# Kernel tuning notes

Measured on AMD Instinct MI355X. Metric: run time of the kernel, lower is better.

## Reference

```python
import jax, jax.numpy as jnp
import numpy as np

N, E, DIN, DOUT = 50000, 800000, 256, 256
P = DOUT // 2  # attention projection dim = feature_dim // 2


def _mlp2(x, W1, b1, W2, b2):
    # nn.Sequential(Linear, ReLU, Linear)
    return jax.nn.relu(x @ W1 + b1) @ W2 + b2


def _spmm(indices, values, x):
    # y[r] = sum_e values[e] * x[col[e]] for edges with row[e] == r
    rows, cols = indices[0], indices[1]
    return jax.ops.segment_sum(values[:, None] * x[cols], rows, num_segments=x.shape[0])


def setup_inputs() -> dict:
    key = jax.random.key(0)
    ks = iter(jax.random.split(key, 64))

    def nrm(shape, scale=0.05):
        return jax.random.normal(next(ks), shape, jnp.float32) * scale

    inp = {}
    inp["features"] = jax.random.normal(next(ks), (N, DIN), jnp.float32)
    inp["edge_features"] = jax.random.normal(next(ks), (N, DOUT), jnp.float32)
    for i in (1, 2, 3, 4):
        inp[f"adj{i}_indices"] = jax.random.randint(next(ks), (2, E), 0, N)
        inp[f"adj{i}_values"] = jax.random.uniform(next(ks), (E,), jnp.float32)
    # feature_transform: Linear(in, out)
    inp["ft_W"] = nrm((DIN, DOUT)); inp["ft_b"] = jnp.zeros((DOUT,), jnp.float32)
    # six 2-layer MLPs: first_order(fo), edge(em), second(so), third(to), fourth(qo), final(m)
    for p in ("fo", "em", "so", "to", "qo", "m"):
        inp[f"{p}_W1"] = nrm((DOUT, DOUT)); inp[f"{p}_b1"] = jnp.zeros((DOUT,), jnp.float32)
        inp[f"{p}_W2"] = nrm((DOUT, DOUT)); inp[f"{p}_b2"] = jnp.zeros((DOUT,), jnp.float32)
    # attention query/key projections to DOUT//2
    inp["q_W"] = nrm((DOUT, P)); inp["q_b"] = jnp.zeros((P,), jnp.float32)
    inp["k_W"] = nrm((DOUT, P)); inp["k_b"] = jnp.zeros((P,), jnp.float32)
    return inp


def reference(features, edge_features,
              adj1_indices, adj1_values, adj2_indices, adj2_values,
              adj3_indices, adj3_values, adj4_indices, adj4_values,
              ft_W, ft_b,
              fo_W1, fo_b1, fo_W2, fo_b2,
              em_W1, em_b1, em_W2, em_b2,
              so_W1, so_b1, so_W2, so_b2,
              to_W1, to_b1, to_W2, to_b2,
              qo_W1, qo_b1, qo_W2, qo_b2,
              m_W1, m_b1, m_W2, m_b2,
              q_W, q_b, k_W, k_b):
    feats = features @ ft_W + ft_b                                    # [N, DOUT]
    # first order: spmm -> MLP, then add spmm of edge-MLP features
    fo = _mlp2(_spmm(adj1_indices, adj1_values, feats), fo_W1, fo_b1, fo_W2, fo_b2)
    ef = _mlp2(edge_features, em_W1, em_b1, em_W2, em_b2)
    fo = fo + _spmm(adj1_indices, adj1_values, ef)
    # higher orders: spmm -> MLP + residual
    so_agg = _spmm(adj2_indices, adj2_values, feats)
    so = _mlp2(so_agg, so_W1, so_b1, so_W2, so_b2) + so_agg
    to_agg = _spmm(adj3_indices, adj3_values, feats)
    to = _mlp2(to_agg, to_W1, to_b1, to_W2, to_b2) + to_agg
    qo_agg = _spmm(adj4_indices, adj4_values, feats)
    qo = _mlp2(qo_agg, qo_W1, qo_b1, qo_W2, qo_b2) + qo_agg
    # attention combination over the 5 feature sets
    all_f = jnp.stack([feats, fo, so, to, qo], axis=1)                # [N, 5, DOUT]
    q = feats @ q_W + q_b                                             # [N, P]
    keys = all_f @ k_W + k_b                                          # [N, 5, P]
    scores = jnp.einsum('np,nkp->nk', q, keys)                        # [N, 5]
    w = jax.nn.softmax(scores, axis=-1)
    combined = jnp.einsum('nk,nkd->nd', w, all_f)                     # [N, DOUT]
    # final MLP (dropout is identity in eval mode)
    return _mlp2(combined, m_W1, m_b1, m_W2, m_b2)
```

## Files before the change

kernel.cpp:

```cpp
#include <hip/hip_runtime.h>


#define DO 256

typedef unsigned short u16;
typedef _Float16 f16;
typedef __attribute__((ext_vector_type(8))) _Float16 f16x8;
typedef __attribute__((ext_vector_type(4))) _Float16 f16x4;
typedef __attribute__((ext_vector_type(4))) float f32x4;


struct WDesc { const float* src; f16* dst; };
struct WPack { WDesc w[13]; };
struct CsrSrc { const int* rows[4]; const int* cols[4]; const float* vals[4]; int E[4]; };

__global__ __launch_bounds__(256) void prep_kernel(
    CsrSrc cs, int* __restrict__ cnt, int NPo, WPack wp,
    const float* __restrict__ qW, const float* __restrict__ kW,
    const float* __restrict__ qb, f16* __restrict__ pdst, float* __restrict__ pb)
{
    int y = blockIdx.y;
    if (y < 4) {
        int e = blockIdx.x * 256 + threadIdx.x;
        if (e < cs.E[y]) atomicAdd(&cnt[(size_t)y * NPo + cs.rows[y][e]], 1);
        return;
    }
    if (y < 17) {
        if (blockIdx.x >= 256) return;
        WDesc d = wp.w[y - 4];
        int idx = blockIdx.x * 256 + threadIdx.x;
        int e  = idx & 7;
        int l  = (idx >> 3) & 63;
        int ks = (idx >> 9) & 7;
        int f  = idx >> 12;
        int c  = (f << 4) | (l & 15);
        int k  = ks * 32 + ((l >> 4) << 3) + e;
        d.dst[idx] = (f16)d.src[k * 256 + c];
        return;
    }
    if (y == 17) {
        if (blockIdx.x >= 256) return;
        int idx = blockIdx.x * 256 + threadIdx.x;
        int e  = idx & 7;
        int l  = (idx >> 3) & 63;
        int ks = (idx >> 9) & 7;
        int f  = idx >> 12;
        int c  = (f << 4) | (l & 15);
        int k  = ks * 32 + ((l >> 4) << 3) + e;
        float s = 0.f;
        #pragma unroll 8
        for (int p = 0; p < 128; ++p) s += qW[k * 128 + p] * kW[c * 128 + p];
        pdst[idx] = (f16)s;
        return;
    }
    if (blockIdx.x != 0) return;
    int c = threadIdx.x;
    float s = 0.f;
    #pragma unroll 8
    for (int p = 0; p < 128; ++p) s += qb[p] * kW[c * 128 + p];
    pb[c] = s;
}

__global__ __launch_bounds__(1024) void scan4_kernel(
    const int* __restrict__ cnt0, int* __restrict__ off0, int N, int NPo)
{
    const int* cnt = cnt0 + (size_t)blockIdx.x * NPo;
    int* off = off0 + (size_t)blockIdx.x * NPo;
    __shared__ int part[1024];
    const int t = threadIdx.x;
    const int chunk = (N + 1023) / 1024;
    const int lo = t * chunk;
    const int hi = min(lo + chunk, N);
    int s = 0;
    for (int i = lo; i < hi; ++i) s += cnt[i];
    part[t] = s;
    __syncthreads();
    for (int d = 1; d < 1024; d <<= 1) {
        int u = (t >= d) ? part[t - d] : 0;
        __syncthreads();
        part[t] += u;
        __syncthreads();
    }
    int running = part[t] - s;
    for (int i = lo; i < hi; ++i) { off[i] = running; running += cnt[i]; }
    if (t == 1023) off[N] = part[1023];
}

static __device__ __forceinline__ void stage_A(
    char* smem, const f16* A, const float* A32, int brow, int N, int tid)
{
    #pragma unroll
    for (int j = 0; j < 8; ++j) {
        int i = tid + j * 256;
        int row = i >> 5, slot = i & 31;
        int srow = brow + row; srow = srow < N ? srow : N - 1;
        f16x8 v;
        if (A32) {
            const float* s = &A32[(size_t)srow * 256 + slot * 8];
            float4 v0 = *(const float4*)s;
            float4 v1 = *(const float4*)(s + 4);
            v = f16x8{(f16)v0.x, (f16)v0.y, (f16)v0.z, (f16)v0.w,
                      (f16)v1.x, (f16)v1.y, (f16)v1.z, (f16)v1.w};
        } else {
            v = *(const f16x8*)&A[(size_t)srow * 256 + slot * 8];
        }
        int db = (row * 512 + slot * 16) ^ ((row & 7) << 4);
        *(f16x8*)(smem + db) = v;
    }
}

static __device__ __forceinline__ void gemm_from_lds(
    const char* smem, const f16* W, f32x4 (&acc)[4][4],
    int wave, int lane, int lrow, int kg)
{
    #pragma unroll
    for (int ks = 0; ks < 8; ++ks) {
        f16x8 ah[4], bh[4];
        #pragma unroll
        for (int m = 0; m < 4; ++m) {
            int ab = ((m * 16 + lrow) * 512 + (ks * 4 + kg) * 16) ^ ((lrow & 7) << 4);
            ah[m] = *(const f16x8*)(smem + ab);
        }
        #pragma unroll
        for (int n = 0; n < 4; ++n)
            bh[n] = *(const f16x8*)&W[(size_t)(((wave * 4 + n) * 8 + ks) << 9) + (lane << 3)];
        #pragma unroll
        for (int m = 0; m < 4; ++m)
            #pragma unroll
            for (int n = 0; n < 4; ++n)
                acc[m][n] = __builtin_amdgcn_mfma_f32_16x16x32_f16(
                                ah[m], bh[n], acc[m][n], 0, 0, 0);
    }
}

static __device__ __forceinline__ void fused_mlp_body(
    char* smem, const f16* A, const float* A32,
    const f16* W1, const float* b1, const f16* W2, const float* b2,
    const f16* Ad, f16* Ch, float* Cf, int N, int brow)
{
    const int tid  = threadIdx.x;
    const int wave = tid >> 6, lane = tid & 63;
    const int lrow = lane & 15, kg = lane >> 4;
    const int wc   = wave * 64;

    stage_A(smem, A, A32, brow, N, tid);
    __syncthreads();

    f32x4 acc[4][4] = {};
    gemm_from_lds(smem, W1, acc, wave, lane, lrow, kg);

    __syncthreads();
    #pragma unroll
    for (int n = 0; n < 4; ++n) {
        int c = wc + n * 16 + lrow;
        float bv = b1[c];
        #pragma unroll
        for (int m = 0; m < 4; ++m)
            #pragma unroll
            for (int j = 0; j < 4; ++j) {
                int rl = m * 16 + kg * 4 + j;
                float v = fmaxf(acc[m][n][j] + bv, 0.f);
                int hb = (rl * 512 + c * 2) ^ ((rl & 7) << 4);
                *(f16*)(smem + hb) = (f16)v;
            }
    }
    __syncthreads();

    #pragma unroll
    for (int m = 0; m < 4; ++m)
        #pragma unroll
        for (int n = 0; n < 4; ++n)
            acc[m][n] = f32x4{0.f, 0.f, 0.f, 0.f};
    gemm_from_lds(smem, W2, acc, wave, lane, lrow, kg);

    #pragma unroll
    for (int n = 0; n < 4; ++n) {
        int c = wc + n * 16 + lrow;
        float bv = b2[c];
        #pragma unroll
        for (int m = 0; m < 4; ++m)
            #pragma unroll
            for (int j = 0; j < 4; ++j) {
                int r = brow + m * 16 + kg * 4 + j;
                if (r >= N) continue;
                size_t o = (size_t)r * 256 + c;
                float v = acc[m][n][j] + bv;
                if (Ad) v += (float)Ad[o];
                if (Cf) Cf[o] = v;
                else    Ch[o] = (f16)v;
            }
    }
}

static __device__ __forceinline__ void gemm1_body(
    char* smem, const float* A32, const f16* W1, const float* b1,
    f16* Ch, int N, int brow)
{
    const int tid  = threadIdx.x;
    const int wave = tid >> 6, lane = tid & 63;
    const int lrow = lane & 15, kg = lane >> 4;
    const int wc   = wave * 64;

    stage_A(smem, nullptr, A32, brow, N, tid);
    __syncthreads();
    f32x4 acc[4][4] = {};
    gemm_from_lds(smem, W1, acc, wave, lane, lrow, kg);

    #pragma unroll
    for (int n = 0; n < 4; ++n) {
        int c = wc + n * 16 + lrow;
        float bv = b1[c];
        #pragma unroll
        for (int m = 0; m < 4; ++m)
            #pragma unroll
            for (int j = 0; j < 4; ++j) {
                int r = brow + m * 16 + kg * 4 + j;
                if (r >= N) continue;
                Ch[(size_t)r * 256 + c] = (f16)(acc[m][n][j] + bv);
            }
    }
}

__global__ __launch_bounds__(256) void stage2_kernel(
    CsrSrc cs, const int* __restrict__ off, int* __restrict__ cur,
    int2* __restrict__ se, int NPo, int Emax,
    const float* __restrict__ features, const float* __restrict__ edge_features,
    const f16* __restrict__ w_ft, const float* __restrict__ ft_b,
    const f16* __restrict__ w_em1, const float* __restrict__ em_b1,
    const f16* __restrict__ w_em2, const float* __restrict__ em_b2,
    f16* __restrict__ F, f16* __restrict__ ef, int N)
{
    __shared__ char smem[32768];
    int y = blockIdx.y;
    if (y < 4) {
        int e = blockIdx.x * 256 + threadIdx.x;
        if (e >= cs.E[y]) return;
        int r = cs.rows[y][e];
        int p = off[(size_t)y * NPo + r] + atomicAdd(&cur[(size_t)y * NPo + r], 1);
        se[(size_t)y * Emax + p] = make_int2(cs.cols[y][e],
                                             __float_as_int(cs.vals[y][e]));
        return;
    }
    int gx = blockIdx.x;
    if (gx >= (N + 63) / 64) return;
    if (y == 4)
        gemm1_body(smem, features, w_ft, ft_b, F, N, gx * 64);
    else
        fused_mlp_body(smem, nullptr, edge_features, w_em1, em_b1, w_em2, em_b2,
                       nullptr, ef, nullptr, N, gx * 64);
}

struct Spmm4 {
    const int* off; const int2* se; int NPo; int Emax;
    const f16* F; const f16* ef;
    f16* agg1; f16* aggef; f16* agg2; f16* agg3; f16* agg4;
};
__global__ __launch_bounds__(256) void spmm4_kernel(Spmm4 s, int N) {
    int a = blockIdx.y;
    int r = blockIdx.x * 4 + (threadIdx.x >> 6);
    if (r >= N) return;
    int lane = threadIdx.x & 63;
    const int* off = s.off + (size_t)a * s.NPo;
    const int2* se = s.se + (size_t)a * s.Emax;
    int e0 = off[r], e1 = off[r + 1];
    size_t yo = (size_t)r * DO + lane * 4;

    if (a == 0) {
        float a0 = 0.f, a1 = 0.f, a2 = 0.f, a3 = 0.f;
        float b0 = 0.f, b1 = 0.f, b2 = 0.f, b3 = 0.f;
        for (int e = e0; e < e1; ++e) {
            int2 ev = se[e];
            int c = ev.x; float v = __int_as_float(ev.y);
            size_t xo = (size_t)c * DO + lane * 4;
            f16x4 x1 = *(const f16x4*)&s.F[xo];
            f16x4 x2 = *(const f16x4*)&s.ef[xo];
            a0 = fmaf(v, (float)x1[0], a0); a1 = fmaf(v, (float)x1[1], a1);
            a2 = fmaf(v, (float)x1[2], a2); a3 = fmaf(v, (float)x1[3], a3);
            b0 = fmaf(v, (float)x2[0], b0); b1 = fmaf(v, (float)x2[1], b1);
            b2 = fmaf(v, (float)x2[2], b2); b3 = fmaf(v, (float)x2[3], b3);
        }
        f16x4 o1 = {(f16)a0, (f16)a1, (f16)a2, (f16)a3};
        f16x4 o2 = {(f16)b0, (f16)b1, (f16)b2, (f16)b3};
        *(f16x4*)&s.agg1[yo]  = o1;
        *(f16x4*)&s.aggef[yo] = o2;
    } else {
        f16* Y = (a == 1) ? s.agg2 : (a == 2) ? s.agg3 : s.agg4;
        float a0 = 0.f, a1 = 0.f, a2 = 0.f, a3 = 0.f;
        int e = e0;
        for (; e + 1 < e1; e += 2) {
            int2 ev0 = se[e], ev1 = se[e + 1];
            float v0 = __int_as_float(ev0.y), v1 = __int_as_float(ev1.y);
            f16x4 x0 = *(const f16x4*)&s.F[(size_t)ev0.x * DO + lane * 4];
            f16x4 x1 = *(const f16x4*)&s.F[(size_t)ev1.x * DO + lane * 4];
            a0 = fmaf(v0, (float)x0[0], a0); a1 = fmaf(v0, (float)x0[1], a1);
            a2 = fmaf(v0, (float)x0[2], a2); a3 = fmaf(v0, (float)x0[3], a3);
            a0 = fmaf(v1, (float)x1[0], a0); a1 = fmaf(v1, (float)x1[1], a1);
            a2 = fmaf(v1, (float)x1[2], a2); a3 = fmaf(v1, (float)x1[3], a3);
        }
        if (e < e1) {
            int2 ev = se[e];
            float v = __int_as_float(ev.y);
            f16x4 x = *(const f16x4*)&s.F[(size_t)ev.x * DO + lane * 4];
            a0 = fmaf(v, (float)x[0], a0); a1 = fmaf(v, (float)x[1], a1);
            a2 = fmaf(v, (float)x[2], a2); a3 = fmaf(v, (float)x[3], a3);
        }
        f16x4 o = {(f16)a0, (f16)a1, (f16)a2, (f16)a3};
        *(f16x4*)&Y[yo] = o;
    }
}

struct Mlp4 {
    const f16* a[4]; const f16* ad[4];
    const f16* w1[4]; const f16* w2[4];
    const float* b1[4]; const float* b2[4];
    f16* out[4];
};
__global__ __launch_bounds__(256) void mlp4_kernel(Mlp4 p, int N) {
    __shared__ char smem[32768];
    int y = blockIdx.y;
    fused_mlp_body(smem, p.a[y], nullptr, p.w1[y], p.b1[y], p.w2[y], p.b2[y],
                   p.ad[y], p.out[y], nullptr, N, blockIdx.x * 64);
}

__global__ __launch_bounds__(256) void mlp_kernel(
    const f16* __restrict__ A,
    const f16* __restrict__ W1, const float* __restrict__ b1,
    const f16* __restrict__ W2, const float* __restrict__ b2,
    float* __restrict__ Cf, int N)
{
    __shared__ char smem[32768];
    fused_mlp_body(smem, A, nullptr, W1, b1, W2, b2, nullptr, nullptr, Cf, N,
                   blockIdx.x * 64);
}

__global__ __launch_bounds__(256) void score_combine_kernel(
    const f16* __restrict__ F, const f16* __restrict__ P,
    const float* __restrict__ pb,
    const f16* __restrict__ F1, const f16* __restrict__ F2,
    const f16* __restrict__ F3, const f16* __restrict__ F4,
    f16* __restrict__ O, int N)
{
    __shared__ char smem[32768];
    __shared__ float sred[4][64][5];
    __shared__ float w5[64][5];

    const int tid  = threadIdx.x;
    const int wave = tid >> 6, lane = tid & 63;
    const int lrow = lane & 15, kg = lane >> 4;
    const int wc   = wave * 64;
    const int brow = blockIdx.x * 64;

    stage_A(smem, F, nullptr, brow, N, tid);
    __syncthreads();

    f32x4 acc[4][4] = {};
    gemm_from_lds(smem, P, acc, wave, lane, lrow, kg);

    #pragma unroll
    for (int m = 0; m < 4; ++m) {
        #pragma unroll
        for (int j = 0; j < 4; ++j) {
            int rl = m * 16 + kg * 4 + j;
            int r  = brow + rl;
            float p0 = 0.f, p1 = 0.f, p2 = 0.f, p3 = 0.f, p4 = 0.f;
            if (r < N) {
                #pragma unroll
                for (int n = 0; n < 4; ++n) {
                    int c = wc + n * 16 + lrow;
                    float v = acc[m][n][j] + pb[c];
                    int ab = (rl * 512 + c * 2) ^ ((rl & 7) << 4);
                    float f0 = (float)*(const f16*)(smem + ab);
                    size_t fo = (size_t)r * 256 + c;
                    p0 += v * f0;
                    p1 += v * (float)F1[fo];
                    p2 += v * (float)F2[fo];
                    p3 += v * (float)F3[fo];
                    p4 += v * (float)F4[fo];
                }
            }
            #pragma unroll
            for (int d = 1; d < 16; d <<= 1) {
                p0 += __shfl_xor(p0, d, 64);
                p1 += __shfl_xor(p1, d, 64);
                p2 += __shfl_xor(p2, d, 64);
                p3 += __shfl_xor(p3, d, 64);
                p4 += __shfl_xor(p4, d, 64);
            }
            if (lrow == 0) {
                sred[wave][rl][0] = p0; sred[wave][rl][1] = p1;
                sred[wave][rl][2] = p2; sred[wave][rl][3] = p3;
                sred[wave][rl][4] = p4;
            }
        }
    }
    __syncthreads();

    if (tid < 64) {
        float s[5];
        #pragma unroll
        for (int k = 0; k < 5; ++k)
            s[k] = sred[0][tid][k] + sred[1][tid][k] + sred[2][tid][k] + sred[3][tid][k];
        float mx = fmaxf(fmaxf(fmaxf(s[0], s[1]), fmaxf(s[2], s[3])), s[4]);
        float sum = 0.f;
        #pragma unroll
        for (int k = 0; k < 5; ++k) { s[k] = expf(s[k] - mx); sum += s[k]; }
        float inv = 1.f / sum;
        #pragma unroll
        for (int k = 0; k < 5; ++k) w5[tid][k] = s[k] * inv;
    }
    __syncthreads();

    #pragma unroll
    for (int m = 0; m < 4; ++m) {
        #pragma unroll
        for (int j = 0; j < 4; ++j) {
            int rl = m * 16 + kg * 4 + j;
            int r  = brow + rl;
            if (r >= N) continue;
            float w0 = w5[rl][0], w1 = w5[rl][1], w2 = w5[rl][2],
                  w3 = w5[rl][3], w4 = w5[rl][4];
            #pragma unroll
            for (int n = 0; n < 4; ++n) {
                int c = wc + n * 16 + lrow;
                int ab = (rl * 512 + c * 2) ^ ((rl & 7) << 4);
                float f0 = (float)*(const f16*)(smem + ab);
                size_t fo = (size_t)r * 256 + c;
                float res = w0 * f0
                          + w1 * (float)F1[fo]
                          + w2 * (float)F2[fo]
                          + w3 * (float)F3[fo]
                          + w4 * (float)F4[fo];
                O[fo] = (f16)res;
            }
        }
    }
}

extern "C" void kernel_launch(void* const* d_in, const int* in_sizes, int n_in,
                              void* d_out, int out_size, void* d_ws, size_t ws_size,
                              hipStream_t stream)
{
    const float* features      = (const float*)d_in[0];
    const float* edge_features = (const float*)d_in[1];
    CsrSrc cs;
    for (int i = 0; i < 4; ++i) {
        const int* idx = (const int*)d_in[2 + 2 * i];
        cs.E[i]    = in_sizes[3 + 2 * i];
        cs.rows[i] = idx;
        cs.cols[i] = idx + cs.E[i];
        cs.vals[i] = (const float*)d_in[3 + 2 * i];
    }
    const int Emax = max(max(cs.E[0], cs.E[1]), max(cs.E[2], cs.E[3]));

    const float* ft_W = (const float*)d_in[10]; const float* ft_b = (const float*)d_in[11];
    const float* fo_W1 = (const float*)d_in[12]; const float* fo_b1 = (const float*)d_in[13];
    const float* fo_W2 = (const float*)d_in[14]; const float* fo_b2 = (const float*)d_in[15];
    const float* em_W1 = (const float*)d_in[16]; const float* em_b1 = (const float*)d_in[17];
    const float* em_W2 = (const float*)d_in[18]; const float* em_b2 = (const float*)d_in[19];
    const float* so_W1 = (const float*)d_in[20]; const float* so_b1 = (const float*)d_in[21];
    const float* so_W2 = (const float*)d_in[22]; const float* so_b2 = (const float*)d_in[23];
    const float* to_W1 = (const float*)d_in[24]; const float* to_b1 = (const float*)d_in[25];
    const float* to_W2 = (const float*)d_in[26]; const float* to_b2 = (const float*)d_in[27];
    const float* qo_W1 = (const float*)d_in[28]; const float* qo_b1 = (const float*)d_in[29];
    const float* qo_W2 = (const float*)d_in[30]; const float* qo_b2 = (const float*)d_in[31];
    const float* m_W1  = (const float*)d_in[32]; const float* m_b1  = (const float*)d_in[33];
    const float* m_W2  = (const float*)d_in[34]; const float* m_b2  = (const float*)d_in[35];
    const float* q_W   = (const float*)d_in[36]; const float* q_b   = (const float*)d_in[37];
    const float* k_W   = (const float*)d_in[38]; const float* k_b   = (const float*)d_in[39];
    (void)k_b;

    const int N = in_sizes[0] / 256;
    const size_t NS = (size_t)N * DO;

    char* base = (char*)d_ws;
    size_t o = 0;
    auto take = [&](size_t bytes) { char* p = base + o; o += (bytes + 63) & ~(size_t)63; return p; };
    const int NPo = (N + 64) & ~63;
    int*  cnt = (int*)take((size_t)4 * NPo * 4);
    int*  cur = (int*)take((size_t)4 * NPo * 4);
    int*  off = (int*)take((size_t)4 * NPo * 4);
    int2* se  = (int2*)take((size_t)4 * Emax * 8);
    f16* B1 = (f16*)take(NS * 2);
    f16* B2 = (f16*)take(NS * 2);
    f16* B3 = (f16*)take(NS * 2);
    f16* B4 = (f16*)take(NS * 2);
    f16* B5 = (f16*)take(NS * 2);
    f16* B6 = (f16*)take(NS * 2);
    const size_t WSQ = 65536;
    f16* WT = (f16*)take(14 * WSQ * 2);
    float* pb = (float*)take(256 * 4);
    if (o > ws_size) return;

    f16* F  = B4;
    f16* OT = (f16*)d_out;

    f16* w[14];
    for (int i = 0; i < 14; ++i) w[i] = WT + (size_t)i * WSQ;

    dim3 blk(256);
    const int EG = (Emax + 255) / 256;
    const int GG = (N + 63) / 64;

    hipMemsetAsync(cnt, 0, (size_t)8 * NPo * 4, stream);

    {
        WPack wp;
        const float* src[13] = {ft_W, fo_W1, fo_W2, em_W1, em_W2, so_W1, so_W2,
                                to_W1, to_W2, qo_W1, qo_W2, m_W1, m_W2};
        for (int i = 0; i < 13; ++i) { wp.w[i].src = src[i]; wp.w[i].dst = w[i]; }
        hipLaunchKernelGGL(prep_kernel, dim3(EG, 19), blk, 0, stream,
                           cs, cnt, NPo, wp, q_W, k_W, q_b, w[13], pb);
    }
    hipLaunchKernelGGL(scan4_kernel, dim3(4), dim3(1024), 0, stream, cnt, off, N, NPo);
    hipLaunchKernelGGL(stage2_kernel, dim3(EG, 6), blk, 0, stream,
                       cs, off, cur, se, NPo, Emax,
                       features, edge_features,
                       w[0], ft_b, w[3], em_b1, w[4], em_b2, F, B3, N);
    {
        Spmm4 sp;
        sp.off = off; sp.se = se; sp.NPo = NPo; sp.Emax = Emax;
        sp.F = F; sp.ef = B3;
        sp.agg1 = B1; sp.aggef = B2; sp.agg2 = B5; sp.agg3 = B6; sp.agg4 = OT;
        hipLaunchKernelGGL(spmm4_kernel, dim3((N + 3) / 4, 4), blk, 0, stream, sp, N);
    }
    {
        Mlp4 p;
        const f16* a[4]  = {B1, B5, B6, OT};
        const f16* ad[4] = {B2, B5, B6, OT};
        f16* out[4]      = {B1, B5, B6, OT};
        int wi1[4] = {1, 5, 7, 9}, wi2[4] = {2, 6, 8, 10};
        const float* bb1[4] = {fo_b1, so_b1, to_b1, qo_b1};
        const float* bb2[4] = {fo_b2, so_b2, to_b2, qo_b2};
        for (int i = 0; i < 4; ++i) {
            p.a[i] = a[i]; p.ad[i] = ad[i]; p.out[i] = out[i];
            p.w1[i] = w[wi1[i]]; p.w2[i] = w[wi2[i]];
            p.b1[i] = bb1[i]; p.b2[i] = bb2[i];
        }
        hipLaunchKernelGGL(mlp4_kernel, dim3(GG, 4), blk, 0, stream, p, N);
    }
    hipLaunchKernelGGL(score_combine_kernel, dim3(GG), blk, 0, stream,
                       F, w[13], pb, B1, B5, B6, OT, B1, N);
    hipLaunchKernelGGL(mlp_kernel, dim3(GG), blk, 0, stream,
                       B1, w[11], m_b1, w[12], m_b2, (float*)d_out, N);
}
```

Before: 1.112 ms.

## Fuse attention combine with final MLP and split SpMM into five uniform slices

```diff
diff --git a/kernel.cpp b/kernel.cpp
--- a/kernel.cpp
+++ b/kernel.cpp
@@ -133,22 +133,12 @@
     }
 }
 
-static __device__ __forceinline__ void fused_mlp_body(
-    char* smem, const f16* A, const float* A32,
-    const f16* W1, const float* b1, const f16* W2, const float* b2,
-    const f16* Ad, f16* Ch, float* Cf, int N, int brow)
-{
-    const int tid  = threadIdx.x;
-    const int wave = tid >> 6, lane = tid & 63;
-    const int lrow = lane & 15, kg = lane >> 4;
-    const int wc   = wave * 64;
-
-    stage_A(smem, A, A32, brow, N, tid);
-    __syncthreads();
-
-    f32x4 acc[4][4] = {};
+static __device__ __forceinline__ void mlp_from_lds(
+    char* smem, const f16* W1, const float* b1, const f16* W2,
+    f32x4 (&acc)[4][4], int wave, int lane, int lrow, int kg)
+{
+    const int wc = wave * 64;
     gemm_from_lds(smem, W1, acc, wave, lane, lrow, kg);
-
     __syncthreads();
     #pragma unroll
     for (int n = 0; n < 4; ++n) {
@@ -165,13 +155,29 @@
             }
     }
     __syncthreads();
-
     #pragma unroll
     for (int m = 0; m < 4; ++m)
         #pragma unroll
         for (int n = 0; n < 4; ++n)
             acc[m][n] = f32x4{0.f, 0.f, 0.f, 0.f};
     gemm_from_lds(smem, W2, acc, wave, lane, lrow, kg);
+}
+
+static __device__ __forceinline__ void fused_mlp_body(
+    char* smem, const f16* A, const float* A32,
+    const f16* W1, const float* b1, const f16* W2, const float* b2,
+    const f16* Ad, f16* Ch, float* Cf, int N, int brow)
+{
+    const int tid  = threadIdx.x;
+    const int wave = tid >> 6, lane = tid & 63;
+    const int lrow = lane & 15, kg = lane >> 4;
+    const int wc   = wave * 64;
+
+    stage_A(smem, A, A32, brow, N, tid);
+    __syncthreads();
+
+    f32x4 acc[4][4] = {};
+    mlp_from_lds(smem, W1, b1, W2, acc, wave, lane, lrow, kg);
 
     #pragma unroll
     for (int n = 0; n < 4; ++n) {
@@ -250,63 +256,51 @@
                        nullptr, ef, nullptr, N, gx * 64);
 }
 
-struct Spmm4 {
+struct Spmm5 {
     const int* off; const int2* se; int NPo; int Emax;
     const f16* F; const f16* ef;
-    f16* agg1; f16* aggef; f16* agg2; f16* agg3; f16* agg4;
+    f16* out[5];
 };
-__global__ __launch_bounds__(256) void spmm4_kernel(Spmm4 s, int N) {
-    int a = blockIdx.y;
+__global__ __launch_bounds__(256) void spmm5_kernel(Spmm5 s, int N) {
+    int y = blockIdx.y;
     int r = blockIdx.x * 4 + (threadIdx.x >> 6);
     if (r >= N) return;
     int lane = threadIdx.x & 63;
+    int a = (y <= 1) ? 0 : y - 1;
     const int* off = s.off + (size_t)a * s.NPo;
     const int2* se = s.se + (size_t)a * s.Emax;
+    const f16* X = (y == 1) ? s.ef : s.F;
+    f16* Y = s.out[y];
     int e0 = off[r], e1 = off[r + 1];
-    size_t yo = (size_t)r * DO + lane * 4;
-
-    if (a == 0) {
-        float a0 = 0.f, a1 = 0.f, a2 = 0.f, a3 = 0.f;
-        float b0 = 0.f, b1 = 0.f, b2 = 0.f, b3 = 0.f;
-        for (int e = e0; e < e1; ++e) {
-            int2 ev = se[e];
-            int c = ev.x; float v = __int_as_float(ev.y);
-            size_t xo = (size_t)c * DO + lane * 4;
-            f16x4 x1 = *(const f16x4*)&s.F[xo];
-            f16x4 x2 = *(const f16x4*)&s.ef[xo];
-            a0 = fmaf(v, (float)x1[0], a0); a1 = fmaf(v, (float)x1[1], a1);
-            a2 = fmaf(v, (float)x1[2], a2); a3 = fmaf(v, (float)x1[3], a3);
-            b0 = fmaf(v, (float)x2[0], b0); b1 = fmaf(v, (float)x2[1], b1);
-            b2 = fmaf(v, (float)x2[2], b2); b3 = fmaf(v, (float)x2[3], b3);
-        }
-        f16x4 o1 = {(f16)a0, (f16)a1, (f16)a2, (f16)a3};
-        f16x4 o2 = {(f16)b0, (f16)b1, (f16)b2, (f16)b3};
-        *(f16x4*)&s.agg1[yo]  = o1;
-        *(f16x4*)&s.aggef[yo] = o2;
-    } else {
-        f16* Y = (a == 1) ? s.agg2 : (a == 2) ? s.agg3 : s.agg4;
-        float a0 = 0.f, a1 = 0.f, a2 = 0.f, a3 = 0.f;
-        int e = e0;
-        for (; e + 1 < e1; e += 2) {
-            int2 ev0 = se[e], ev1 = se[e + 1];
-            float v0 = __int_as_float(ev0.y), v1 = __int_as_float(ev1.y);
-            f16x4 x0 = *(const f16x4*)&s.F[(size_t)ev0.x * DO + lane * 4];
-            f16x4 x1 = *(const f16x4*)&s.F[(size_t)ev1.x * DO + lane * 4];
-            a0 = fmaf(v0, (float)x0[0], a0); a1 = fmaf(v0, (float)x0[1], a1);
-            a2 = fmaf(v0, (float)x0[2], a2); a3 = fmaf(v0, (float)x0[3], a3);
-            a0 = fmaf(v1, (float)x1[0], a0); a1 = fmaf(v1, (float)x1[1], a1);
-            a2 = fmaf(v1, (float)x1[2], a2); a3 = fmaf(v1, (float)x1[3], a3);
-        }
-        if (e < e1) {
-            int2 ev = se[e];
-            float v = __int_as_float(ev.y);
-            f16x4 x = *(const f16x4*)&s.F[(size_t)ev.x * DO + lane * 4];
-            a0 = fmaf(v, (float)x[0], a0); a1 = fmaf(v, (float)x[1], a1);
-            a2 = fmaf(v, (float)x[2], a2); a3 = fmaf(v, (float)x[3], a3);
-        }
-        f16x4 o = {(f16)a0, (f16)a1, (f16)a2, (f16)a3};
-        *(f16x4*)&Y[yo] = o;
-    }
+
+    float a0 = 0.f, a1 = 0.f, a2 = 0.f, a3 = 0.f;
+    int e = e0;
+    for (; e + 3 < e1; e += 4) {
+        int2 ev0 = se[e], ev1 = se[e + 1], ev2 = se[e + 2], ev3 = se[e + 3];
+        f16x4 x0 = *(const f16x4*)&X[(size_t)ev0.x * DO + lane * 4];
+        f16x4 x1 = *(const f16x4*)&X[(size_t)ev1.x * DO + lane * 4];
+        f16x4 x2 = *(const f16x4*)&X[(size_t)ev2.x * DO + lane * 4];
+        f16x4 x3 = *(const f16x4*)&X[(size_t)ev3.x * DO + lane * 4];
+        float v0 = __int_as_float(ev0.y), v1 = __int_as_float(ev1.y);
+        float v2 = __int_as_float(ev2.y), v3 = __int_as_float(ev3.y);
+        a0 = fmaf(v0, (float)x0[0], a0); a1 = fmaf(v0, (float)x0[1], a1);
+        a2 = fmaf(v0, (float)x0[2], a2); a3 = fmaf(v0, (float)x0[3], a3);
+        a0 = fmaf(v1, (float)x1[0], a0); a1 = fmaf(v1, (float)x1[1], a1);
+        a2 = fmaf(v1, (float)x1[2], a2); a3 = fmaf(v1, (float)x1[3], a3);
+        a0 = fmaf(v2, (float)x2[0], a0); a1 = fmaf(v2, (float)x2[1], a1);
+        a2 = fmaf(v2, (float)x2[2], a2); a3 = fmaf(v2, (float)x2[3], a3);
+        a0 = fmaf(v3, (float)x3[0], a0); a1 = fmaf(v3, (float)x3[1], a1);
+        a2 = fmaf(v3, (float)x3[2], a2); a3 = fmaf(v3, (float)x3[3], a3);
+    }
+    for (; e < e1; ++e) {
+        int2 ev = se[e];
+        float v = __int_as_float(ev.y);
+        f16x4 x = *(const f16x4*)&X[(size_t)ev.x * DO + lane * 4];
+        a0 = fmaf(v, (float)x[0], a0); a1 = fmaf(v, (float)x[1], a1);
+        a2 = fmaf(v, (float)x[2], a2); a3 = fmaf(v, (float)x[3], a3);
+    }
+    f16x4 o = {(f16)a0, (f16)a1, (f16)a2, (f16)a3};
+    *(f16x4*)&Y[(size_t)r * DO + lane * 4] = o;
 }
 
 struct Mlp4 {
@@ -322,23 +316,14 @@
                    p.ad[y], p.out[y], nullptr, N, blockIdx.x * 64);
 }
 
-__global__ __launch_bounds__(256) void mlp_kernel(
-    const f16* __restrict__ A,
-    const f16* __restrict__ W1, const float* __restrict__ b1,
-    const f16* __restrict__ W2, const float* __restrict__ b2,
-    float* __restrict__ Cf, int N)
-{
-    __shared__ char smem[32768];
-    fused_mlp_body(smem, A, nullptr, W1, b1, W2, b2, nullptr, nullptr, Cf, N,
-                   blockIdx.x * 64);
-}
-
-__global__ __launch_bounds__(256) void score_combine_kernel(
+__global__ __launch_bounds__(256) void score_combine_mlp_kernel(
     const f16* __restrict__ F, const f16* __restrict__ P,
     const float* __restrict__ pb,
     const f16* __restrict__ F1, const f16* __restrict__ F2,
     const f16* __restrict__ F3, const f16* __restrict__ F4,
-    f16* __restrict__ O, int N)
+    const f16* __restrict__ mW1, const float* __restrict__ mb1,
+    const f16* __restrict__ mW2, const float* __restrict__ mb2,
+    float* __restrict__ Out, int N)
 {
     __shared__ char smem[32768];
     __shared__ float sred[4][64][5];
@@ -416,7 +401,6 @@
         for (int j = 0; j < 4; ++j) {
             int rl = m * 16 + kg * 4 + j;
             int r  = brow + rl;
-            if (r >= N) continue;
             float w0 = w5[rl][0], w1 = w5[rl][1], w2 = w5[rl][2],
                   w3 = w5[rl][3], w4 = w5[rl][4];
             #pragma unroll
@@ -424,15 +408,40 @@
                 int c = wc + n * 16 + lrow;
                 int ab = (rl * 512 + c * 2) ^ ((rl & 7) << 4);
                 float f0 = (float)*(const f16*)(smem + ab);
-                size_t fo = (size_t)r * 256 + c;
-                float res = w0 * f0
-                          + w1 * (float)F1[fo]
-                          + w2 * (float)F2[fo]
-                          + w3 * (float)F3[fo]
-                          + w4 * (float)F4[fo];
-                O[fo] = (f16)res;
+                float res = f0;
+                if (r < N) {
+                    size_t fo = (size_t)r * 256 + c;
+                    res = w0 * f0
+                        + w1 * (float)F1[fo]
+                        + w2 * (float)F2[fo]
+                        + w3 * (float)F3[fo]
+                        + w4 * (float)F4[fo];
+                }
+                *(f16*)(smem + ab) = (f16)res;
             }
         }
+    }
+    __syncthreads();
+
+    #pragma unroll
+    for (int m = 0; m < 4; ++m)
+        #pragma unroll
+        for (int n = 0; n < 4; ++n)
+            acc[m][n] = f32x4{0.f, 0.f, 0.f, 0.f};
+    mlp_from_lds(smem, mW1, mb1, mW2, acc, wave, lane, lrow, kg);
+
+    #pragma unroll
+    for (int n = 0; n < 4; ++n) {
+        int c = wc + n * 16 + lrow;
+        float bv = mb2[c];
+        #pragma unroll
+        for (int m = 0; m < 4; ++m)
+            #pragma unroll
+            for (int j = 0; j < 4; ++j) {
+                int r = brow + m * 16 + kg * 4 + j;
+                if (r >= N) continue;
+                Out[(size_t)r * 256 + c] = acc[m][n][j] + bv;
+            }
     }
 }
 
@@ -486,13 +495,13 @@
     f16* B4 = (f16*)take(NS * 2);
     f16* B5 = (f16*)take(NS * 2);
     f16* B6 = (f16*)take(NS * 2);
+    f16* B7 = (f16*)take(NS * 2);
     const size_t WSQ = 65536;
     f16* WT = (f16*)take(14 * WSQ * 2);
     float* pb = (float*)take(256 * 4);
     if (o > ws_size) return;
 
-    f16* F  = B4;
-    f16* OT = (f16*)d_out;
+    f16* F = B4;
 
     f16* w[14];
     for (int i = 0; i < 14; ++i) w[i] = WT + (size_t)i * WSQ;
@@ -517,17 +526,17 @@
                        features, edge_features,
                        w[0], ft_b, w[3], em_b1, w[4], em_b2, F, B3, N);
     {
-        Spmm4 sp;
+        Spmm5 sp;
         sp.off = off; sp.se = se; sp.NPo = NPo; sp.Emax = Emax;
         sp.F = F; sp.ef = B3;
-        sp.agg1 = B1; sp.aggef = B2; sp.agg2 = B5; sp.agg3 = B6; sp.agg4 = OT;
-        hipLaunchKernelGGL(spmm4_kernel, dim3((N + 3) / 4, 4), blk, 0, stream, sp, N);
+        sp.out[0] = B1; sp.out[1] = B2; sp.out[2] = B5; sp.out[3] = B6; sp.out[4] = B7;
+        hipLaunchKernelGGL(spmm5_kernel, dim3((N + 3) / 4, 5), blk, 0, stream, sp, N);
     }
     {
         Mlp4 p;
-        const f16* a[4]  = {B1, B5, B6, OT};
-        const f16* ad[4] = {B2, B5, B6, OT};
-        f16* out[4]      = {B1, B5, B6, OT};
+        const f16* a[4]  = {B1, B5, B6, B7};
+        const f16* ad[4] = {B2, B5, B6, B7};
+        f16* out[4]      = {B1, B5, B6, B7};
         int wi1[4] = {1, 5, 7, 9}, wi2[4] = {2, 6, 8, 10};
         const float* bb1[4] = {fo_b1, so_b1, to_b1, qo_b1};
         const float* bb2[4] = {fo_b2, so_b2, to_b2, qo_b2};
@@ -538,8 +547,7 @@
         }
         hipLaunchKernelGGL(mlp4_kernel, dim3(GG, 4), blk, 0, stream, p, N);
     }
-    hipLaunchKernelGGL(score_combine_kernel, dim3(GG), blk, 0, stream,
-                       F, w[13], pb, B1, B5, B6, OT, B1, N);
-    hipLaunchKernelGGL(mlp_kernel, dim3(GG), blk, 0, stream,
-                       B1, w[11], m_b1, w[12], m_b2, (float*)d_out, N);
-}
+    hipLaunchKernelGGL(score_combine_mlp_kernel, dim3(GG), blk, 0, stream,
+                       F, w[13], pb, B1, B5, B6, B7,
+                       w[11], m_b1, w[12], m_b2, (float*)d_out, N);
+}
```

Result: faster. 1.075 ms (-3.3%).
